# Performance work log

Measured on AMD Instinct MI355X. Metric: run time of the kernel, lower is better.

Reference implementation:

```python
import jax, jax.numpy as jnp
import numpy as np

N = 65536        # total nodes (32 graphs x 2048 nodes)
E = 1048576      # total edges (avg degree 16)
D = 64           # in_dim
H = 64           # hidden_dim
O = 32           # out_dim
B = 32           # number of graphs in the batch
NPG = 2048       # nodes per graph
EPS = 1e-5
SLOPE = 0.01     # LeakyReLU negative slope


def setup_inputs() -> dict:
    key = jax.random.key(0)
    ks = jax.random.split(key, 7)
    x = jax.random.normal(ks[0], (N, D), jnp.float32)
    edge_weights = jax.random.uniform(ks[1], (E,), jnp.float32)
    src = jax.random.randint(ks[2], (E,), 0, N, dtype=jnp.int32)
    dst = jax.random.randint(ks[3], (E,), 0, N, dtype=jnp.int32)
    graph_ids = (jnp.arange(N, dtype=jnp.int32) // NPG).astype(jnp.int32)
    # DGL GraphConv weight is (in_feats, out_feats); Linear weight is (out, in)
    W1 = jax.random.normal(ks[4], (D, H), jnp.float32) * np.float32(1.0 / np.sqrt(D))
    W2 = jax.random.normal(ks[5], (H, H), jnp.float32) * np.float32(1.0 / np.sqrt(H))
    Wc = jax.random.normal(ks[6], (O, H), jnp.float32) * np.float32(1.0 / np.sqrt(H))
    gn1_w = jnp.ones((H,), jnp.float32); gn1_b = jnp.zeros((H,), jnp.float32); gn1_a = jnp.ones((H,), jnp.float32)
    gn2_w = jnp.ones((H,), jnp.float32); gn2_b = jnp.zeros((H,), jnp.float32); gn2_a = jnp.ones((H,), jnp.float32)
    return dict(x=x, edge_weights=edge_weights, W1=W1, W2=W2, Wc=Wc,
                gn1_w=gn1_w, gn1_b=gn1_b, gn1_a=gn1_a,
                gn2_w=gn2_w, gn2_b=gn2_b, gn2_a=gn2_a,
                src=src, dst=dst, graph_ids=graph_ids)


def _graph_conv(h, W, src, dst, ew, inv_sqrt_out, inv_sqrt_in):
    # DGL GraphConv norm='both' with edge_weight:
    # out = D_in^{-1/2} * scatter_sum( ew * (D_out^{-1/2} h W)[src] -> dst )
    h = (h * inv_sqrt_out[:, None]) @ W                       # [N,H]
    m = h[src] * ew[:, None]                                  # [E,H] gather + edge weight
    agg = jax.ops.segment_sum(m, dst, num_segments=N)         # [N,H] scatter
    return agg * inv_sqrt_in[:, None]


def _graph_norm(x, w, b, a):
    # GraphNorm: (x - a*mean) / sqrt(var(x - a*mean) + eps) * w + b, stats over node dim
    mean = jnp.mean(x, axis=0, keepdims=True)
    sub = x - a * mean
    std = jnp.sqrt(jnp.mean(sub * sub, axis=0, keepdims=True) + EPS)
    return w * (sub / std) + b


def _leaky(x):
    return jnp.where(x >= 0, x, SLOPE * x)


def reference(x, edge_weights, W1, W2, Wc,
              gn1_w, gn1_b, gn1_a, gn2_w, gn2_b, gn2_a,
              src, dst, graph_ids):
    ones_e = jnp.ones((E,), x.dtype)
    deg_out = jnp.maximum(jax.ops.segment_sum(ones_e, src, num_segments=N), 1.0)
    deg_in = jnp.maximum(jax.ops.segment_sum(ones_e, dst, num_segments=N), 1.0)
    inv_so = jax.lax.rsqrt(deg_out)
    inv_si = jax.lax.rsqrt(deg_in)

    h = _graph_conv(x, W1, src, dst, edge_weights, inv_so, inv_si)
    h = _graph_norm(_leaky(h), gn1_w, gn1_b, gn1_a)
    h = _graph_conv(h, W2, src, dst, edge_weights, inv_so, inv_si)
    h = _graph_norm(_leaky(h), gn2_w, gn2_b, gn2_a)

    # dgl.mean_nodes: per-graph mean pooling
    counts = jax.ops.segment_sum(jnp.ones((N,), x.dtype), graph_ids, num_segments=B)
    pooled = jax.ops.segment_sum(h, graph_ids, num_segments=B) / counts[:, None]  # [B,H]
    return pooled @ Wc.T  # [B,O]
```

## Files before the change

### kernel.cpp

```cpp
#include <hip/hip_runtime.h>

#define N_NODES 65536
#define N_EDGES 1048576
#define B_GRAPHS 32
#define NPG     2048
#define EPS_GN  1e-5f
#define SLOPE   0.01f
#define NBUCKET 512
#define STRIDE_B 2432

typedef unsigned short ushort_t;
typedef unsigned int uint_t;

static __device__ __forceinline__ ushort_t f2bf(float f) {
    uint_t u = __float_as_uint(f);
    return (ushort_t)((u + 0x7FFFu + ((u >> 16) & 1u)) >> 16);
}

static __device__ __forceinline__ void acc_bf8(float4& a0, float4& a1, uint4 u, float w) {
    a0.x += __uint_as_float(u.x << 16) * w;
    a0.y += __uint_as_float(u.x & 0xffff0000u) * w;
    a0.z += __uint_as_float(u.y << 16) * w;
    a0.w += __uint_as_float(u.y & 0xffff0000u) * w;
    a1.x += __uint_as_float(u.z << 16) * w;
    a1.y += __uint_as_float(u.z & 0xffff0000u) * w;
    a1.z += __uint_as_float(u.w << 16) * w;
    a1.w += __uint_as_float(u.w & 0xffff0000u) * w;
}

__global__ __launch_bounds__(256) void hist_kernel(const int4* __restrict__ src4,
                                                   unsigned int* __restrict__ partial,
                                                   int* __restrict__ cursor) {
    __shared__ unsigned int bins[16384];
    int tid = threadIdx.x, c = blockIdx.x;
#pragma unroll
    for (int k = 0; k < 64; ++k) bins[k * 256 + tid] = 0u;
    if (c == 0) {
        cursor[tid] = tid * STRIDE_B;
        cursor[256 + tid] = (256 + tid) * STRIDE_B;
    }
    __syncthreads();
#pragma unroll
    for (int k = 0; k < 16; ++k) {
        int4 v = src4[c * 4096 + k * 256 + tid];
        atomicAdd(&bins[v.x >> 2], 1u << ((v.x & 3) * 8));
        atomicAdd(&bins[v.y >> 2], 1u << ((v.y & 3) * 8));
        atomicAdd(&bins[v.z >> 2], 1u << ((v.z & 3) * 8));
        atomicAdd(&bins[v.w >> 2], 1u << ((v.w & 3) * 8));
    }
    __syncthreads();
    unsigned int* dstp = partial + c * 16384;
#pragma unroll
    for (int k = 0; k < 64; ++k) dstp[k * 256 + tid] = bins[k * 256 + tid];
}

__global__ __launch_bounds__(256) void reduce_src(const unsigned int* __restrict__ partial,
                                                  float4* __restrict__ inv_so4) {
    int w = blockIdx.x * 256 + threadIdx.x;
    unsigned int s0 = 0, s1 = 0, s2 = 0, s3 = 0;
#pragma unroll
    for (int c = 0; c < 64; ++c) {
        unsigned int v = partial[c * 16384 + w];
        s0 += v & 255u; s1 += (v >> 8) & 255u; s2 += (v >> 16) & 255u; s3 += v >> 24;
    }
    float4 r;
    r.x = rsqrtf((float)max((int)s0, 1));
    r.y = rsqrtf((float)max((int)s1, 1));
    r.z = rsqrtf((float)max((int)s2, 1));
    r.w = rsqrtf((float)max((int)s3, 1));
    inv_so4[w] = r;
}

__global__ __launch_bounds__(256) void bucket_scatter(const int4* __restrict__ src4,
                                                      const int4* __restrict__ dst4,
                                                      const float4* __restrict__ ew4,
                                                      int* __restrict__ cursor,
                                                      int2* __restrict__ bedges) {
    __shared__ int lhist[NBUCKET];
    __shared__ int lstart[NBUCKET];
    __shared__ int gbase[NBUCKET];
    __shared__ int scA[256], scB[256];
    __shared__ int2 staged[4096];
    int tid = threadIdx.x;
    int vbase = blockIdx.x * 1024;
    lhist[tid] = 0;
    lhist[tid + 256] = 0;
    __syncthreads();
    int w0[16]; int wbr[16]; float wwt[16];
#pragma unroll
    for (int k = 0; k < 4; ++k) {
        int4 s = src4[vbase + k * 256 + tid];
        int4 d = dst4[vbase + k * 256 + tid];
        float4 w = ew4[vbase + k * 256 + tid];
        int ss[4] = {s.x, s.y, s.z, s.w};
        int dd[4] = {d.x, d.y, d.z, d.w};
        float wf[4] = {w.x, w.y, w.z, w.w};
#pragma unroll
        for (int j = 0; j < 4; ++j) {
            int b = dd[j] >> 7;
            w0[k * 4 + j] = ss[j] | ((dd[j] & 127) << 16);
            wwt[k * 4 + j] = wf[j];
            int r = atomicAdd(&lhist[b], 1);
            wbr[k * 4 + j] = (b << 16) | r;
        }
    }
    __syncthreads();
    int cntA = lhist[tid], cntB = lhist[tid + 256];
    scA[tid] = cntA;
    scB[tid] = cntB;
    __syncthreads();
    for (int off = 1; off < 256; off <<= 1) {
        int tA = (tid >= off) ? scA[tid - off] : 0;
        int tB = (tid >= off) ? scB[tid - off] : 0;
        __syncthreads();
        scA[tid] += tA;
        scB[tid] += tB;
        __syncthreads();
    }
    int lowtot = scA[255];
    lstart[tid] = scA[tid] - cntA;
    lstart[tid + 256] = lowtot + scB[tid] - cntB;
    gbase[tid] = cntA ? atomicAdd(&cursor[tid], cntA) : 0;
    gbase[tid + 256] = cntB ? atomicAdd(&cursor[tid + 256], cntB) : 0;
    __syncthreads();
#pragma unroll
    for (int k = 0; k < 16; ++k)
        staged[lstart[wbr[k] >> 16] + (wbr[k] & 0xFFFF)] =
            make_int2(w0[k], __float_as_int(wwt[k]));
    __syncthreads();
    {
        int gb = gbase[tid], ls = lstart[tid];
        for (int i = 0; i < cntA; ++i) bedges[gb + i] = staged[ls + i];
        gb = gbase[tid + 256]; ls = lstart[tid + 256];
        for (int i = 0; i < cntB; ++i) bedges[gb + i] = staged[ls + i];
    }
}

__global__ __launch_bounds__(256) void refine_lite(const int* __restrict__ bedges_x,
                                                   const int* __restrict__ cursor,
                                                   int* __restrict__ nstart,
                                                   int* __restrict__ ndeg) {
    __shared__ int hist[128], sc[128];
    int tid = threadIdx.x, b = blockIdx.x;
    int e0 = b * STRIDE_B;
    int nE = cursor[b] - e0;
    if (tid < 128) hist[tid] = 0;
    __syncthreads();
    for (int i = tid; i < nE; i += 256)
        atomicAdd(&hist[(bedges_x[2 * (e0 + i)] >> 16) & 127], 1);
    __syncthreads();
    if (tid < 128) sc[tid] = hist[tid];
    __syncthreads();
    for (int off = 1; off < 128; off <<= 1) {
        int t = (tid >= off && tid < 128) ? sc[tid - off] : 0;
        __syncthreads();
        if (tid < 128) sc[tid] += t;
        __syncthreads();
    }
    if (tid < 128) {
        int cnt = hist[tid];
        nstart[b * 128 + tid] = sc[tid] - cnt;
        ndeg[b * 128 + tid] = cnt;
    }
}

__global__ __launch_bounds__(256) void gemm_f32(const float* __restrict__ in,
                                                const float* __restrict__ W,
                                                const float* __restrict__ inv_so,
                                                ushort_t* __restrict__ out_bf) {
    __shared__ float wT[64][68];
    __shared__ float xlds[64][64];
    int tid = threadIdx.x;
#pragma unroll
    for (int j = 0; j < 16; ++j) {
        int i = j * 256 + tid;
        wT[i & 63][i >> 6] = W[i];
    }
    int r0 = blockIdx.x * 64;
#pragma unroll
    for (int j = 0; j < 16; ++j) {
        int i = j * 256 + tid;
        int r = i >> 6, k = i & 63;
        int gr = r0 + r;
        xlds[r][k] = in[(size_t)gr * 64 + k] * inv_so[gr];
    }
    __syncthreads();
    int c = tid & 63;
    int rg = tid >> 6;
    float acc[16];
#pragma unroll
    for (int j = 0; j < 16; ++j) acc[j] = 0.f;
#pragma unroll
    for (int k0 = 0; k0 < 64; k0 += 4) {
        float4 wv = *(const float4*)&wT[c][k0];
#pragma unroll
        for (int j = 0; j < 16; ++j) {
            float4 xv = *(const float4*)&xlds[rg * 16 + j][k0];
            acc[j] += xv.x * wv.x + xv.y * wv.y + xv.z * wv.z + xv.w * wv.w;
        }
    }
#pragma unroll
    for (int j = 0; j < 16; ++j)
        out_bf[(size_t)(r0 + rg * 16 + j) * 64 + c] = f2bf(acc[j]);
}

__global__ __launch_bounds__(256) void gemm_bf16(const ushort_t* __restrict__ in,
                                                 const float* __restrict__ W,
                                                 const float* __restrict__ inv_so,
                                                 const float* __restrict__ alpha,
                                                 const float* __restrict__ beta,
                                                 ushort_t* __restrict__ out_bf) {
    __shared__ float wT[64][68];
    __shared__ float xlds[64][64];
    int tid = threadIdx.x;
#pragma unroll
    for (int j = 0; j < 16; ++j) {
        int i = j * 256 + tid;
        wT[i & 63][i >> 6] = W[i];
    }
    int r0 = blockIdx.x * 64;
    const uint_t* inU = (const uint_t*)in;
#pragma unroll
    for (int j = 0; j < 8; ++j) {
        int idx = j * 256 + tid;
        int r = idx >> 5, kp = idx & 31;
        int gr = r0 + r;
        uint_t u = inU[(size_t)gr * 32 + kp];
        int k0 = kp * 2;
        float lo = __uint_as_float(u << 16);
        float hi = __uint_as_float(u & 0xffff0000u);
        float iso = inv_so[gr];
        xlds[r][k0]     = (alpha[k0] * lo + beta[k0]) * iso;
        xlds[r][k0 + 1] = (alpha[k0 + 1] * hi + beta[k0 + 1]) * iso;
    }
    __syncthreads();
    int c = tid & 63;
    int rg = tid >> 6;
    float acc[16];
#pragma unroll
    for (int j = 0; j < 16; ++j) acc[j] = 0.f;
#pragma unroll
    for (int k0 = 0; k0 < 64; k0 += 4) {
        float4 wv = *(const float4*)&wT[c][k0];
#pragma unroll
        for (int j = 0; j < 16; ++j) {
            float4 xv = *(const float4*)&xlds[rg * 16 + j][k0];
            acc[j] += xv.x * wv.x + xv.y * wv.y + xv.z * wv.z + xv.w * wv.w;
        }
    }
#pragma unroll
    for (int j = 0; j < 16; ++j)
        out_bf[(size_t)(r0 + rg * 16 + j) * 64 + c] = f2bf(acc[j]);
}

__global__ __launch_bounds__(1024, 8) void agg_bucket(const ushort_t* __restrict__ Tb,
                                                      const int2* __restrict__ bedges,
                                                      const int* __restrict__ cursor,
                                                      const int* __restrict__ nstart,
                                                      const int* __restrict__ ndeg,
                                                      ushort_t* __restrict__ Yb,
                                                      float4* __restrict__ statsP4) {
    __shared__ int2 sorted[STRIDE_B];
    __shared__ int nst[128], ndg[128], scur[128];
    int tid = threadIdx.x, b = blockIdx.x;
    int e0 = b * STRIDE_B;
    int nE = cursor[b] - e0;
    if (tid < 128) {
        int st = nstart[b * 128 + tid];
        nst[tid] = st;
        scur[tid] = st;
        ndg[tid] = ndeg[b * 128 + tid];
    }
    __syncthreads();
    for (int i = tid; i < nE; i += 1024) {
        int2 e = bedges[e0 + i];
        int dl = (e.x >> 16) & 127;
        int pos = atomicAdd(&scur[dl], 1);
        sorted[pos] = make_int2(e.x & 0xFFFF, e.y);
    }
    __syncthreads();
    const long* sl = (const long*)sorted;
    int l8 = tid & 7;
    int nl = tid >> 3;
    int node = b * 128 + nl;
    int off = nst[nl];
    int cnt = ndg[nl];
    float4 a0 = make_float4(0.f, 0.f, 0.f, 0.f);
    float4 a1 = make_float4(0.f, 0.f, 0.f, 0.f);
    int i = 0;
    for (; i + 8 <= cnt; i += 8) {
        long e[8];
#pragma unroll
        for (int k = 0; k < 8; ++k) e[k] = sl[off + i + k];
        uint4 t[8];
#pragma unroll
        for (int k = 0; k < 8; ++k)
            t[k] = ((const uint4*)(Tb + (((size_t)(e[k] & 0xFFFF)) << 6)))[l8];
#pragma unroll
        for (int k = 0; k < 8; ++k)
            acc_bf8(a0, a1, t[k], __int_as_float((int)(e[k] >> 32)));
    }
    for (; i < cnt; ++i) {
        long e = sl[off + i];
        uint4 u = ((const uint4*)(Tb + (((size_t)(e & 0xFFFF)) << 6)))[l8];
        acc_bf8(a0, a1, u, __int_as_float((int)(e >> 32)));
    }
    float s = rsqrtf((float)max(cnt, 1));
    float4 v0, v1;
    v0.x = a0.x * s; v0.x = (v0.x >= 0.f) ? v0.x : SLOPE * v0.x;
    v0.y = a0.y * s; v0.y = (v0.y >= 0.f) ? v0.y : SLOPE * v0.y;
    v0.z = a0.z * s; v0.z = (v0.z >= 0.f) ? v0.z : SLOPE * v0.z;
    v0.w = a0.w * s; v0.w = (v0.w >= 0.f) ? v0.w : SLOPE * v0.w;
    v1.x = a1.x * s; v1.x = (v1.x >= 0.f) ? v1.x : SLOPE * v1.x;
    v1.y = a1.y * s; v1.y = (v1.y >= 0.f) ? v1.y : SLOPE * v1.y;
    v1.z = a1.z * s; v1.z = (v1.z >= 0.f) ? v1.z : SLOPE * v1.z;
    v1.w = a1.w * s; v1.w = (v1.w >= 0.f) ? v1.w : SLOPE * v1.w;
    if (Yb) {
        uint_t p0 = (uint_t)f2bf(v0.x) | ((uint_t)f2bf(v0.y) << 16);
        uint_t p1 = (uint_t)f2bf(v0.z) | ((uint_t)f2bf(v0.w) << 16);
        uint_t p2 = (uint_t)f2bf(v1.x) | ((uint_t)f2bf(v1.y) << 16);
        uint_t p3 = (uint_t)f2bf(v1.z) | ((uint_t)f2bf(v1.w) << 16);
        ((uint4*)Yb)[(size_t)node * 8 + l8] = make_uint4(p0, p1, p2, p3);
    }
    float4 s0 = v0, s1 = v1;
    float4 q0 = make_float4(v0.x * v0.x, v0.y * v0.y, v0.z * v0.z, v0.w * v0.w);
    float4 q1 = make_float4(v1.x * v1.x, v1.y * v1.y, v1.z * v1.z, v1.w * v1.w);
#pragma unroll
    for (int m = 8; m <= 32; m <<= 1) {
        s0.x += __shfl_xor(s0.x, m); s0.y += __shfl_xor(s0.y, m);
        s0.z += __shfl_xor(s0.z, m); s0.w += __shfl_xor(s0.w, m);
        s1.x += __shfl_xor(s1.x, m); s1.y += __shfl_xor(s1.y, m);
        s1.z += __shfl_xor(s1.z, m); s1.w += __shfl_xor(s1.w, m);
        q0.x += __shfl_xor(q0.x, m); q0.y += __shfl_xor(q0.y, m);
        q0.z += __shfl_xor(q0.z, m); q0.w += __shfl_xor(q0.w, m);
        q1.x += __shfl_xor(q1.x, m); q1.y += __shfl_xor(q1.y, m);
        q1.z += __shfl_xor(q1.z, m); q1.w += __shfl_xor(q1.w, m);
    }
    int wv = tid >> 6, ln = tid & 63;
    if (ln < 8) {
        float4* row = statsP4 + ((size_t)b * 16 + wv) * 32;
        row[ln * 2 + 0] = s0;
        row[ln * 2 + 1] = s1;
        row[16 + ln * 2 + 0] = q0;
        row[16 + ln * 2 + 1] = q1;
    }
}

__global__ __launch_bounds__(256) void reduce_statsA(const float* __restrict__ statsP,
                                                     float* __restrict__ slab) {
    __shared__ float red[256];
    int tid = threadIdx.x, b = blockIdx.x;
    int col = tid & 127, half = tid >> 7;
    float s = 0.f;
    for (int i = half; i < 128; i += 2)
        s += statsP[(size_t)(b * 128 + i) * 128 + col];
    red[tid] = s;
    __syncthreads();
    if (tid < 128) slab[b * 128 + tid] = red[tid] + red[tid + 128];
}

__global__ __launch_bounds__(256) void reduce_stats2(const float* __restrict__ statsP,
                                                     float* __restrict__ slab,
                                                     float* __restrict__ pooledSum) {
    __shared__ float red[256];
    int tid = threadIdx.x, b = blockIdx.x;
    if (b < 64) {
        int col = tid & 127, half = tid >> 7;
        float s = 0.f;
        for (int i = half; i < 128; i += 2)
            s += statsP[(size_t)(b * 128 + i) * 128 + col];
        red[tid] = s;
        __syncthreads();
        if (tid < 128) slab[b * 128 + tid] = red[tid] + red[tid + 128];
    } else {
        int g = b - 64;
        int col = tid & 63, part = tid >> 6;
        float s = 0.f;
        for (int r = g * 256 + part; r < (g + 1) * 256; r += 4)
            s += statsP[(size_t)r * 128 + col];
        red[tid] = s;
        __syncthreads();
        if (tid < 64)
            pooledSum[g * 64 + tid] =
                red[tid] + red[tid + 64] + red[tid + 128] + red[tid + 192];
    }
}

__global__ void finalize_kernel(const float* __restrict__ slab,
                                const float* __restrict__ w, const float* __restrict__ b,
                                const float* __restrict__ a,
                                float* __restrict__ alpha, float* __restrict__ beta) {
    int f = threadIdx.x;
    float Sy = 0.f, Qy = 0.f;
    for (int i = 0; i < 64; ++i) {
        Sy += slab[i * 128 + f];
        Qy += slab[i * 128 + 64 + f];
    }
    float m = Sy * (1.f / N_NODES);
    float q = Qy * (1.f / N_NODES);
    float af = a[f];
    float var = q - 2.f * af * m * m + af * af * m * m;
    float al = w[f] / sqrtf(var + EPS_GN);
    alpha[f] = al;
    beta[f] = b[f] - al * af * m;
}

__global__ __launch_bounds__(256) void out_kernel(const float* __restrict__ slab2,
                                                  const float* __restrict__ gn_w,
                                                  const float* __restrict__ gn_b,
                                                  const float* __restrict__ gn_a,
                                                  const float* __restrict__ pooledSum,
                                                  const float* __restrict__ Wc,
                                                  float* __restrict__ out) {
    __shared__ float al[64], be[64];
    __shared__ float p[B_GRAPHS * 64];
    int tid = threadIdx.x;
    if (tid < 64) {
        float Sy = 0.f, Qy = 0.f;
        for (int i = 0; i < 64; ++i) {
            Sy += slab2[i * 128 + tid];
            Qy += slab2[i * 128 + 64 + tid];
        }
        float m = Sy * (1.f / N_NODES);
        float q = Qy * (1.f / N_NODES);
        float af = gn_a[tid];
        float var = q - 2.f * af * m * m + af * af * m * m;
        float a_ = gn_w[tid] / sqrtf(var + EPS_GN);
        al[tid] = a_;
        be[tid] = gn_b[tid] - a_ * af * m;
    }
    __syncthreads();
    for (int i = tid; i < B_GRAPHS * 64; i += 256) {
        int f = i & 63;
        p[i] = al[f] * (pooledSum[i] * (1.f / NPG)) + be[f];
    }
    __syncthreads();
    for (int idx = tid; idx < B_GRAPHS * 32; idx += 256) {
        int g = idx >> 5, o = idx & 31;
        float acc = 0.f;
        for (int f = 0; f < 64; ++f)
            acc += p[g * 64 + f] * Wc[o * 64 + f];
        out[idx] = acc;
    }
}

extern "C" void kernel_launch(void* const* d_in, const int* in_sizes, int n_in,
                              void* d_out, int out_size, void* d_ws, size_t ws_size,
                              hipStream_t stream) {
    const float* x     = (const float*)d_in[0];
    const float* ew    = (const float*)d_in[1];
    const float* W1    = (const float*)d_in[2];
    const float* W2    = (const float*)d_in[3];
    const float* Wc    = (const float*)d_in[4];
    const float* gn1_w = (const float*)d_in[5];
    const float* gn1_b = (const float*)d_in[6];
    const float* gn1_a = (const float*)d_in[7];
    const float* gn2_w = (const float*)d_in[8];
    const float* gn2_b = (const float*)d_in[9];
    const float* gn2_a = (const float*)d_in[10];
    const int* src     = (const int*)d_in[11];
    const int* dst     = (const int*)d_in[12];

    char* ws = (char*)d_ws;
    int*   cursor    = (int*)(ws + 0);
    float* ab1       = (float*)(ws + 4096);
    float* pooledSum = (float*)(ws + 8192);
    float* slab1     = (float*)(ws + 16384);
    float* slab2     = (float*)(ws + 49152);
    int*   nstart    = (int*)(ws + 131072);
    int*   ndeg      = (int*)(ws + 393216);
    float* inv_so    = (float*)(ws + 655360);
    unsigned int* partial = (unsigned int*)(ws + (2u << 20));
    int2*  bedges    = (int2*)(ws + (10u << 20));
    ushort_t* Tbf    = (ushort_t*)(ws + (20u << 20));
    ushort_t* Ybf    = (ushort_t*)(ws + (28u << 20));
    float* statsP    = (float*)(ws + (36u << 20));

    hist_kernel<<<64, 256, 0, stream>>>((const int4*)src, partial, cursor);
    reduce_src<<<64, 256, 0, stream>>>(partial, (float4*)inv_so);
    bucket_scatter<<<256, 256, 0, stream>>>((const int4*)src, (const int4*)dst,
                                            (const float4*)ew, cursor, bedges);
    refine_lite<<<NBUCKET, 256, 0, stream>>>((const int*)bedges, cursor, nstart, ndeg);

    gemm_f32<<<N_NODES / 64, 256, 0, stream>>>(x, W1, inv_so, Tbf);
    agg_bucket<<<NBUCKET, 1024, 0, stream>>>(Tbf, bedges, cursor, nstart, ndeg,
                                             Ybf, (float4*)statsP);
    reduce_statsA<<<64, 256, 0, stream>>>(statsP, slab1);
    finalize_kernel<<<1, 64, 0, stream>>>(slab1, gn1_w, gn1_b, gn1_a, ab1 + 0, ab1 + 64);

    gemm_bf16<<<N_NODES / 64, 256, 0, stream>>>(Ybf, W2, inv_so, ab1 + 0, ab1 + 64, Tbf);
    agg_bucket<<<NBUCKET, 1024, 0, stream>>>(Tbf, bedges, cursor, nstart, ndeg,
                                             nullptr, (float4*)statsP);
    reduce_stats2<<<96, 256, 0, stream>>>(statsP, slab2, pooledSum);

    out_kernel<<<1, 256, 0, stream>>>(slab2, gn2_w, gn2_b, gn2_a, pooledSum, Wc,
                                      (float*)d_out);
}
```

Baseline: 155.3 us.

## Split bf16 feature tables into two 32-column planes and fuse finalize kernels

Stores the bf16 node feature tables as two 32-feature planes. The aggregation kernel now runs two passes, one per plane, with a block barrier between them, so each pass gathers from a smaller 4 MB working set that is more likely to stay in cache. It also folds the GraphNorm finalize and output kernels into the preceding reduction kernels using a last-block atomic counter, which removes two launches. The cost is that the edge list is read twice, and the stats layout and gemm load and store indexing change to match the planes.

```diff
diff --git a/kernel.cpp b/kernel.cpp
--- a/kernel.cpp
+++ b/kernel.cpp
@@ -8,6 +8,7 @@
 #define SLOPE   0.01f
 #define NBUCKET 512
 #define STRIDE_B 2432
+#define PLANE   ((size_t)N_NODES * 32)
 
 typedef unsigned short ushort_t;
 typedef unsigned int uint_t;
@@ -17,20 +18,17 @@
     return (ushort_t)((u + 0x7FFFu + ((u >> 16) & 1u)) >> 16);
 }
 
-static __device__ __forceinline__ void acc_bf8(float4& a0, float4& a1, uint4 u, float w) {
-    a0.x += __uint_as_float(u.x << 16) * w;
-    a0.y += __uint_as_float(u.x & 0xffff0000u) * w;
-    a0.z += __uint_as_float(u.y << 16) * w;
-    a0.w += __uint_as_float(u.y & 0xffff0000u) * w;
-    a1.x += __uint_as_float(u.z << 16) * w;
-    a1.y += __uint_as_float(u.z & 0xffff0000u) * w;
-    a1.z += __uint_as_float(u.w << 16) * w;
-    a1.w += __uint_as_float(u.w & 0xffff0000u) * w;
+static __device__ __forceinline__ void acc_bf4(float4& a, uint2 u, float w) {
+    a.x += __uint_as_float(u.x << 16) * w;
+    a.y += __uint_as_float(u.x & 0xffff0000u) * w;
+    a.z += __uint_as_float(u.y << 16) * w;
+    a.w += __uint_as_float(u.y & 0xffff0000u) * w;
 }
 
 __global__ __launch_bounds__(256) void hist_kernel(const int4* __restrict__ src4,
                                                    unsigned int* __restrict__ partial,
-                                                   int* __restrict__ cursor) {
+                                                   int* __restrict__ cursor,
+                                                   int* __restrict__ done) {
     __shared__ unsigned int bins[16384];
     int tid = threadIdx.x, c = blockIdx.x;
 #pragma unroll
@@ -38,6 +36,7 @@
     if (c == 0) {
         cursor[tid] = tid * STRIDE_B;
         cursor[256 + tid] = (256 + tid) * STRIDE_B;
+        if (tid < 2) done[tid] = 0;
     }
     __syncthreads();
 #pragma unroll
@@ -187,6 +186,7 @@
     __syncthreads();
     int c = tid & 63;
     int rg = tid >> 6;
+    ushort_t* outp = out_bf + (size_t)(c >> 5) * PLANE + (c & 31);
     float acc[16];
 #pragma unroll
     for (int j = 0; j < 16; ++j) acc[j] = 0.f;
@@ -201,7 +201,7 @@
     }
 #pragma unroll
     for (int j = 0; j < 16; ++j)
-        out_bf[(size_t)(r0 + rg * 16 + j) * 64 + c] = f2bf(acc[j]);
+        outp[(size_t)(r0 + rg * 16 + j) * 32] = f2bf(acc[j]);
 }
 
 __global__ __launch_bounds__(256) void gemm_bf16(const ushort_t* __restrict__ in,
@@ -225,8 +225,9 @@
         int idx = j * 256 + tid;
         int r = idx >> 5, kp = idx & 31;
         int gr = r0 + r;
-        uint_t u = inU[(size_t)gr * 32 + kp];
-        int k0 = kp * 2;
+        int pl = kp >> 4, kw = kp & 15;
+        uint_t u = inU[(size_t)pl * (PLANE / 2) + (size_t)gr * 16 + kw];
+        int k0 = pl * 32 + kw * 2;
         float lo = __uint_as_float(u << 16);
         float hi = __uint_as_float(u & 0xffff0000u);
         float iso = inv_so[gr];
@@ -236,6 +237,7 @@
     __syncthreads();
     int c = tid & 63;
     int rg = tid >> 6;
+    ushort_t* outp = out_bf + (size_t)(c >> 5) * PLANE + (c & 31);
     float acc[16];
 #pragma unroll
     for (int j = 0; j < 16; ++j) acc[j] = 0.f;
@@ -250,7 +252,7 @@
     }
 #pragma unroll
     for (int j = 0; j < 16; ++j)
-        out_bf[(size_t)(r0 + rg * 16 + j) * 64 + c] = f2bf(acc[j]);
+        outp[(size_t)(r0 + rg * 16 + j) * 32] = f2bf(acc[j]);
 }
 
 __global__ __launch_bounds__(1024, 8) void agg_bucket(const ushort_t* __restrict__ Tb,
@@ -285,46 +287,53 @@
     int node = b * 128 + nl;
     int off = nst[nl];
     int cnt = ndg[nl];
-    float4 a0 = make_float4(0.f, 0.f, 0.f, 0.f);
-    float4 a1 = make_float4(0.f, 0.f, 0.f, 0.f);
-    int i = 0;
-    for (; i + 8 <= cnt; i += 8) {
-        long e[8];
-#pragma unroll
-        for (int k = 0; k < 8; ++k) e[k] = sl[off + i + k];
-        uint4 t[8];
-#pragma unroll
-        for (int k = 0; k < 8; ++k)
-            t[k] = ((const uint4*)(Tb + (((size_t)(e[k] & 0xFFFF)) << 6)))[l8];
-#pragma unroll
-        for (int k = 0; k < 8; ++k)
-            acc_bf8(a0, a1, t[k], __int_as_float((int)(e[k] >> 32)));
-    }
-    for (; i < cnt; ++i) {
-        long e = sl[off + i];
-        uint4 u = ((const uint4*)(Tb + (((size_t)(e & 0xFFFF)) << 6)))[l8];
-        acc_bf8(a0, a1, u, __int_as_float((int)(e >> 32)));
+    float4 vA, vB;
+#pragma unroll
+    for (int pass = 0; pass < 2; ++pass) {
+        const ushort_t* Tp = Tb + (size_t)pass * PLANE;
+        float4 a = make_float4(0.f, 0.f, 0.f, 0.f);
+        int i = 0;
+        for (; i + 8 <= cnt; i += 8) {
+            long e[8];
+#pragma unroll
+            for (int k = 0; k < 8; ++k) e[k] = sl[off + i + k];
+            uint2 t[8];
+#pragma unroll
+            for (int k = 0; k < 8; ++k)
+                t[k] = ((const uint2*)(Tp + (((size_t)(e[k] & 0xFFFF)) << 5)))[l8];
+#pragma unroll
+            for (int k = 0; k < 8; ++k)
+                acc_bf4(a, t[k], __int_as_float((int)(e[k] >> 32)));
+        }
+        for (; i < cnt; ++i) {
+            long e = sl[off + i];
+            uint2 u = ((const uint2*)(Tp + (((size_t)(e & 0xFFFF)) << 5)))[l8];
+            acc_bf4(a, u, __int_as_float((int)(e >> 32)));
+        }
+        if (pass == 0) vA = a; else vB = a;
+        __syncthreads();
     }
     float s = rsqrtf((float)max(cnt, 1));
-    float4 v0, v1;
-    v0.x = a0.x * s; v0.x = (v0.x >= 0.f) ? v0.x : SLOPE * v0.x;
-    v0.y = a0.y * s; v0.y = (v0.y >= 0.f) ? v0.y : SLOPE * v0.y;
-    v0.z = a0.z * s; v0.z = (v0.z >= 0.f) ? v0.z : SLOPE * v0.z;
-    v0.w = a0.w * s; v0.w = (v0.w >= 0.f) ? v0.w : SLOPE * v0.w;
-    v1.x = a1.x * s; v1.x = (v1.x >= 0.f) ? v1.x : SLOPE * v1.x;
-    v1.y = a1.y * s; v1.y = (v1.y >= 0.f) ? v1.y : SLOPE * v1.y;
-    v1.z = a1.z * s; v1.z = (v1.z >= 0.f) ? v1.z : SLOPE * v1.z;
-    v1.w = a1.w * s; v1.w = (v1.w >= 0.f) ? v1.w : SLOPE * v1.w;
+    vA.x *= s; vA.x = (vA.x >= 0.f) ? vA.x : SLOPE * vA.x;
+    vA.y *= s; vA.y = (vA.y >= 0.f) ? vA.y : SLOPE * vA.y;
+    vA.z *= s; vA.z = (vA.z >= 0.f) ? vA.z : SLOPE * vA.z;
+    vA.w *= s; vA.w = (vA.w >= 0.f) ? vA.w : SLOPE * vA.w;
+    vB.x *= s; vB.x = (vB.x >= 0.f) ? vB.x : SLOPE * vB.x;
+    vB.y *= s; vB.y = (vB.y >= 0.f) ? vB.y : SLOPE * vB.y;
+    vB.z *= s; vB.z = (vB.z >= 0.f) ? vB.z : SLOPE * vB.z;
+    vB.w *= s; vB.w = (vB.w >= 0.f) ? vB.w : SLOPE * vB.w;
     if (Yb) {
-        uint_t p0 = (uint_t)f2bf(v0.x) | ((uint_t)f2bf(v0.y) << 16);
-        uint_t p1 = (uint_t)f2bf(v0.z) | ((uint_t)f2bf(v0.w) << 16);
-        uint_t p2 = (uint_t)f2bf(v1.x) | ((uint_t)f2bf(v1.y) << 16);
-        uint_t p3 = (uint_t)f2bf(v1.z) | ((uint_t)f2bf(v1.w) << 16);
-        ((uint4*)Yb)[(size_t)node * 8 + l8] = make_uint4(p0, p1, p2, p3);
-    }
-    float4 s0 = v0, s1 = v1;
-    float4 q0 = make_float4(v0.x * v0.x, v0.y * v0.y, v0.z * v0.z, v0.w * v0.w);
-    float4 q1 = make_float4(v1.x * v1.x, v1.y * v1.y, v1.z * v1.z, v1.w * v1.w);
+        uint2 pa, pb;
+        pa.x = (uint_t)f2bf(vA.x) | ((uint_t)f2bf(vA.y) << 16);
+        pa.y = (uint_t)f2bf(vA.z) | ((uint_t)f2bf(vA.w) << 16);
+        pb.x = (uint_t)f2bf(vB.x) | ((uint_t)f2bf(vB.y) << 16);
+        pb.y = (uint_t)f2bf(vB.z) | ((uint_t)f2bf(vB.w) << 16);
+        ((uint2*)(Yb + ((size_t)node << 5)))[l8] = pa;
+        ((uint2*)(Yb + PLANE + ((size_t)node << 5)))[l8] = pb;
+    }
+    float4 s0 = vA, s1 = vB;
+    float4 q0 = make_float4(vA.x * vA.x, vA.y * vA.y, vA.z * vA.z, vA.w * vA.w);
+    float4 q1 = make_float4(vB.x * vB.x, vB.y * vB.y, vB.z * vB.z, vB.w * vB.w);
 #pragma unroll
     for (int m = 8; m <= 32; m <<= 1) {
         s0.x += __shfl_xor(s0.x, m); s0.y += __shfl_xor(s0.y, m);
@@ -339,16 +348,23 @@
     int wv = tid >> 6, ln = tid & 63;
     if (ln < 8) {
         float4* row = statsP4 + ((size_t)b * 16 + wv) * 32;
-        row[ln * 2 + 0] = s0;
-        row[ln * 2 + 1] = s1;
-        row[16 + ln * 2 + 0] = q0;
-        row[16 + ln * 2 + 1] = q1;
-    }
-}
-
-__global__ __launch_bounds__(256) void reduce_statsA(const float* __restrict__ statsP,
-                                                     float* __restrict__ slab) {
+        row[ln] = s0;
+        row[8 + ln] = s1;
+        row[16 + ln] = q0;
+        row[24 + ln] = q1;
+    }
+}
+
+__global__ __launch_bounds__(256) void reduce_finalize1(const float* __restrict__ statsP,
+                                                        float* __restrict__ slab,
+                                                        const float* __restrict__ w,
+                                                        const float* __restrict__ bb,
+                                                        const float* __restrict__ a,
+                                                        float* __restrict__ alpha,
+                                                        float* __restrict__ beta,
+                                                        int* __restrict__ done) {
     __shared__ float red[256];
+    __shared__ int isLast;
     int tid = threadIdx.x, b = blockIdx.x;
     int col = tid & 127, half = tid >> 7;
     float s = 0.f;
@@ -357,12 +373,36 @@
     red[tid] = s;
     __syncthreads();
     if (tid < 128) slab[b * 128 + tid] = red[tid] + red[tid + 128];
-}
-
-__global__ __launch_bounds__(256) void reduce_stats2(const float* __restrict__ statsP,
-                                                     float* __restrict__ slab,
-                                                     float* __restrict__ pooledSum) {
+    __threadfence();
+    if (tid == 0) isLast = (atomicAdd(done, 1) == 63);
+    __syncthreads();
+    if (isLast && tid < 64) {
+        float Sy = 0.f, Qy = 0.f;
+        for (int i = 0; i < 64; ++i) {
+            Sy += slab[i * 128 + tid];
+            Qy += slab[i * 128 + 64 + tid];
+        }
+        float m = Sy * (1.f / N_NODES);
+        float q = Qy * (1.f / N_NODES);
+        float af = a[tid];
+        float var = q - 2.f * af * m * m + af * af * m * m;
+        float al = w[tid] / sqrtf(var + EPS_GN);
+        alpha[tid] = al;
+        beta[tid] = bb[tid] - al * af * m;
+    }
+}
+
+__global__ __launch_bounds__(256) void reduce_out2(const float* __restrict__ statsP,
+                                                   float* __restrict__ slab,
+                                                   float* __restrict__ pooledSum,
+                                                   const float* __restrict__ gn_w,
+                                                   const float* __restrict__ gn_b,
+                                                   const float* __restrict__ gn_a,
+                                                   const float* __restrict__ Wc,
+                                                   float* __restrict__ out,
+                                                   int* __restrict__ done) {
     __shared__ float red[256];
+    __shared__ int isLast;
     int tid = threadIdx.x, b = blockIdx.x;
     if (b < 64) {
         int col = tid & 127, half = tid >> 7;
@@ -384,42 +424,17 @@
             pooledSum[g * 64 + tid] =
                 red[tid] + red[tid + 64] + red[tid + 128] + red[tid + 192];
     }
-}
-
-__global__ void finalize_kernel(const float* __restrict__ slab,
-                                const float* __restrict__ w, const float* __restrict__ b,
-                                const float* __restrict__ a,
-                                float* __restrict__ alpha, float* __restrict__ beta) {
-    int f = threadIdx.x;
-    float Sy = 0.f, Qy = 0.f;
-    for (int i = 0; i < 64; ++i) {
-        Sy += slab[i * 128 + f];
-        Qy += slab[i * 128 + 64 + f];
-    }
-    float m = Sy * (1.f / N_NODES);
-    float q = Qy * (1.f / N_NODES);
-    float af = a[f];
-    float var = q - 2.f * af * m * m + af * af * m * m;
-    float al = w[f] / sqrtf(var + EPS_GN);
-    alpha[f] = al;
-    beta[f] = b[f] - al * af * m;
-}
-
-__global__ __launch_bounds__(256) void out_kernel(const float* __restrict__ slab2,
-                                                  const float* __restrict__ gn_w,
-                                                  const float* __restrict__ gn_b,
-                                                  const float* __restrict__ gn_a,
-                                                  const float* __restrict__ pooledSum,
-                                                  const float* __restrict__ Wc,
-                                                  float* __restrict__ out) {
+    __threadfence();
+    if (tid == 0) isLast = (atomicAdd(done, 1) == 95);
+    __syncthreads();
+    if (!isLast) return;
     __shared__ float al[64], be[64];
     __shared__ float p[B_GRAPHS * 64];
-    int tid = threadIdx.x;
     if (tid < 64) {
         float Sy = 0.f, Qy = 0.f;
         for (int i = 0; i < 64; ++i) {
-            Sy += slab2[i * 128 + tid];
-            Qy += slab2[i * 128 + 64 + tid];
+            Sy += slab[i * 128 + tid];
+            Qy += slab[i * 128 + 64 + tid];
         }
         float m = Sy * (1.f / N_NODES);
         float q = Qy * (1.f / N_NODES);
@@ -463,6 +478,7 @@
 
     char* ws = (char*)d_ws;
     int*   cursor    = (int*)(ws + 0);
+    int*   done      = (int*)(ws + 2048);
     float* ab1       = (float*)(ws + 4096);
     float* pooledSum = (float*)(ws + 8192);
     float* slab1     = (float*)(ws + 16384);
@@ -476,7 +492,7 @@
     ushort_t* Ybf    = (ushort_t*)(ws + (28u << 20));
     float* statsP    = (float*)(ws + (36u << 20));
 
-    hist_kernel<<<64, 256, 0, stream>>>((const int4*)src, partial, cursor);
+    hist_kernel<<<64, 256, 0, stream>>>((const int4*)src, partial, cursor, done);
     reduce_src<<<64, 256, 0, stream>>>(partial, (float4*)inv_so);
     bucket_scatter<<<256, 256, 0, stream>>>((const int4*)src, (const int4*)dst,
                                             (const float4*)ew, cursor, bedges);
@@ -485,14 +501,12 @@
     gemm_f32<<<N_NODES / 64, 256, 0, stream>>>(x, W1, inv_so, Tbf);
     agg_bucket<<<NBUCKET, 1024, 0, stream>>>(Tbf, bedges, cursor, nstart, ndeg,
                                              Ybf, (float4*)statsP);
-    reduce_statsA<<<64, 256, 0, stream>>>(statsP, slab1);
-    finalize_kernel<<<1, 64, 0, stream>>>(slab1, gn1_w, gn1_b, gn1_a, ab1 + 0, ab1 + 64);
+    reduce_finalize1<<<64, 256, 0, stream>>>(statsP, slab1, gn1_w, gn1_b, gn1_a,
+                                             ab1 + 0, ab1 + 64, done + 0);
 
     gemm_bf16<<<N_NODES / 64, 256, 0, stream>>>(Ybf, W2, inv_so, ab1 + 0, ab1 + 64, Tbf);
     agg_bucket<<<NBUCKET, 1024, 0, stream>>>(Tbf, bedges, cursor, nstart, ndeg,
                                              nullptr, (float4*)statsP);
-    reduce_stats2<<<96, 256, 0, stream>>>(statsP, slab2, pooledSum);
-
-    out_kernel<<<1, 256, 0, stream>>>(slab2, gn2_w, gn2_b, gn2_a, pooledSum, Wc,
-                                      (float*)d_out);
-}
+    reduce_out2<<<96, 256, 0, stream>>>(statsP, slab2, pooledSum,
+                                        gn2_w, gn2_b, gn2_a, Wc, (float*)d_out, done + 1);
+}
```

Result: slower. 174.6 us (+12.4%).
